# Kernel tuning notes

Hardware: AMD Instinct MI355X
Metric: run time of the kernel (lower is better)

The kernel has to match this reference:

```python
import jax, jax.numpy as jnp
import numpy as np

GROUP = 64   # quantization group size (nunchaku W4A4 default)
QMAX = 7.0   # symmetric int4 positive range


def setup_inputs() -> dict:
    key = jax.random.key(0)
    ks = jax.random.split(key, 6)
    T, K, N, R = 256, 3072, 3072, 32
    x = jax.random.normal(ks[0], (T, K), dtype=jnp.float32)
    # int4 weight codes stored as 0..15 (dequant subtracts zero-point 8)
    qweight = jax.random.randint(ks[1], (N, K), 0, 16, dtype=jnp.int32)
    # per-(out_channel, input_group) weight scales, small positive
    wscales = jax.random.uniform(ks[2], (N, K // GROUP), dtype=jnp.float32) * 0.02 + 1e-3
    lora_down = jax.random.normal(ks[3], (R, K), dtype=jnp.float32) / np.sqrt(K)
    lora_up = jax.random.normal(ks[4], (N, R), dtype=jnp.float32) / np.sqrt(R)
    bias = jax.random.normal(ks[5], (N,), dtype=jnp.float32) * 0.01
    return {"x": x, "qweight": qweight, "wscales": wscales,
            "lora_down": lora_down, "lora_up": lora_up, "bias": bias}


def _quantize_act(x):
    # per-token, per-group symmetric int4 fake-quant (quantize -> dequantize)
    T, K = x.shape
    xg = x.reshape(T, K // GROUP, GROUP)
    scale = jnp.maximum(jnp.max(jnp.abs(xg), axis=-1, keepdims=True) / QMAX, 1e-8)
    q = jnp.clip(jnp.round(xg / scale), -8.0, QMAX)
    return (q * scale).reshape(T, K)


def reference(x, qweight, wscales, lora_down, lora_up, bias):
    # Dequantize int4 weights: (code - 8) * per-group scale  -> [N, K]
    N, K = qweight.shape
    w = (qweight.astype(jnp.float32) - 8.0).reshape(N, K // GROUP, GROUP)
    w = (w * wscales[:, :, None]).reshape(N, K)
    # W4A4 main path: int4-quantized activations x dequantized int4 weights
    x_dq = _quantize_act(x)
    main = x_dq @ w.T                               # [T, N]
    # fused low-rank (SVDQuant LoRA) branch on full-precision activations
    lora = (x @ lora_down.T) @ lora_up.T            # [T, R] @ [R, N]
    return main + lora + bias
```

## Files before the change

### kernel.cpp

```cpp
#include <hip/hip_runtime.h>
#include <stdint.h>

#define T_DIM 256
#define K_DIM 3072
#define N_DIM 3072
#define R_DIM 32
#define KG    48
#define NCHUNK 49
#define NSPLIT 8

typedef __bf16 bf16x8 __attribute__((ext_vector_type(8)));
typedef float  f32x4  __attribute__((ext_vector_type(4)));
typedef unsigned short u16x8 __attribute__((ext_vector_type(8)));

__device__ __forceinline__ unsigned short f2bf(float f) {
    unsigned u = __builtin_bit_cast(unsigned, f);
    unsigned rounding = 0x7FFFu + ((u >> 16) & 1u);
    return (unsigned short)((u + rounding) >> 16);
}

__device__ __forceinline__ bf16x8 cvt8(const float* p) {
    float4 lo = ((const float4*)p)[0], hi = ((const float4*)p)[1];
    u16x8 u;
    u[0] = f2bf(lo.x); u[1] = f2bf(lo.y); u[2] = f2bf(lo.z); u[3] = f2bf(lo.w);
    u[4] = f2bf(hi.x); u[5] = f2bf(hi.y); u[6] = f2bf(hi.z); u[7] = f2bf(hi.w);
    return __builtin_bit_cast(bf16x8, u);
}

__device__ __forceinline__ void glds16(const void* gptr, void* lptr) {
    __builtin_amdgcn_global_load_lds(
        (const __attribute__((address_space(1))) unsigned int*)gptr,
        (__attribute__((address_space(3))) unsigned int*)lptr,
        16, 0, 0);
}

__global__ void build_wtail(const float* __restrict__ lora_up,
                            unsigned short* __restrict__ Wt) {
    int idx = blockIdx.x * 256 + threadIdx.x;
    int n = idx >> 6, j = idx & 63;
    int nblk = n >> 6, nl = n & 63;
    float v = (j < R_DIM) ? lora_up[n * R_DIM + j] : 0.f;
    Wt[(((size_t)nblk * 8 + (j >> 3)) * 64 + nl) * 8 + (j & 7)] = f2bf(v);
}

__global__ __launch_bounds__(256) void quant_act(
        const float* __restrict__ x, unsigned short* __restrict__ Ap) {
    int widx = blockIdx.x * 4 + (threadIdx.x >> 6);
    int lane = threadIdx.x & 63;
    int t = widx / KG, g = widx % KG;
    float v = x[(size_t)t * K_DIM + g * 64 + lane];
    float a = fabsf(v);
    #pragma unroll
    for (int off = 32; off; off >>= 1) a = fmaxf(a, __shfl_xor(a, off));
    float scale = fmaxf(a / 7.0f, 1e-8f);
    float q = rintf(v / scale);
    q = fminf(fmaxf(q, -8.f), 7.f);
    Ap[(((size_t)g * 8 + (lane >> 3)) * 256 + t) * 8 + (lane & 7)] = f2bf(q * scale);
}

__global__ __launch_bounds__(256) void lora_mid(
        const float* __restrict__ x, const float* __restrict__ lora_down,
        float* __restrict__ Lm) {
    int lane = threadIdx.x & 63, wv = threadIdx.x >> 6;
    int mrow = lane & 15, quad = lane >> 4;
    int k0 = blockIdx.x * 32 + quad * 8;
    bf16x8 a[4], b[2];
    #pragma unroll
    for (int mt = 0; mt < 4; ++mt)
        a[mt] = cvt8(x + (size_t)(wv * 64 + mt * 16 + mrow) * K_DIM + k0);
    #pragma unroll
    for (int nt = 0; nt < 2; ++nt)
        b[nt] = cvt8(lora_down + (size_t)(nt * 16 + mrow) * K_DIM + k0);
    f32x4 acc[4][2];
    f32x4 zero = {0.f, 0.f, 0.f, 0.f};
    #pragma unroll
    for (int i = 0; i < 4; ++i) { acc[i][0] = zero; acc[i][1] = zero; }
    #pragma unroll
    for (int mt = 0; mt < 4; ++mt)
        #pragma unroll
        for (int nt = 0; nt < 2; ++nt)
            acc[mt][nt] = __builtin_amdgcn_mfma_f32_16x16x32_bf16(
                a[mt], b[nt], acc[mt][nt], 0, 0, 0);
    #pragma unroll
    for (int mt = 0; mt < 4; ++mt)
        #pragma unroll
        for (int nt = 0; nt < 2; ++nt)
            #pragma unroll
            for (int r = 0; r < 4; ++r)
                atomicAdd(&Lm[(size_t)(wv * 64 + mt * 16 + quad * 4 + r) * R_DIM
                              + nt * 16 + mrow], acc[mt][nt][r]);
}

__global__ void pack_lora(const float* __restrict__ Lm,
                          unsigned short* __restrict__ Ap) {
    int idx = blockIdx.x * 256 + threadIdx.x;
    int t = idx >> 6, j = idx & 63;
    float v = (j < R_DIM) ? Lm[t * R_DIM + j] : 0.f;
    Ap[((size_t)(384 + (j >> 3)) * 256 + t) * 8 + (j & 7)] = f2bf(v);
}

__global__ __launch_bounds__(256) void gemm_main(
        const uint4*          __restrict__ ApU,
        const int*            __restrict__ qweight,
        const float*          __restrict__ wscales,
        const uint4*          __restrict__ WtU,
        const float*          __restrict__ bias,
        float*                __restrict__ out) {
    __shared__ uint4 AsU[2][2048];
    __shared__ uint4 BsU[2][512];
    int nblk  = blockIdx.x;
    int split = blockIdx.y;
    int c0 = split * 6;
    int c1 = (split == NSPLIT - 1) ? NCHUNK : c0 + 6;
    int tid = threadIdx.x;
    int lane = tid & 63, wv = tid >> 6;
    int mrow = lane & 15, quad = lane >> 4;
    int n_row = tid >> 2, seg = tid & 3;
    const int nbase = nblk * 64;
    const int* qrow = qweight + (size_t)(nbase + n_row) * K_DIM + seg * 16;
    const float* wsrow = wscales + (size_t)(nbase + n_row) * KG;

    f32x4 acc[4][4];
    f32x4 zero = {0.f, 0.f, 0.f, 0.f};
    #pragma unroll
    for (int i = 0; i < 4; ++i)
        #pragma unroll
        for (int j = 0; j < 4; ++j) acc[i][j] = zero;

    int4 bc[2][4];
    float wsr[2];

    {
        const uint4* gA = ApU + (size_t)c0 * 2048;
        #pragma unroll
        for (int i = 0; i < 8; ++i)
            glds16(&gA[tid + i * 256], &AsU[0][tid + i * 256]);
        const int4* g0 = (const int4*)(qrow + c0 * 64);
        const int4* g1 = (const int4*)(qrow + (c0 + 1) * 64);
        #pragma unroll
        for (int i = 0; i < 4; ++i) { bc[0][i] = g0[i]; bc[1][i] = g1[i]; }
        wsr[0] = wsrow[c0];
        wsr[1] = wsrow[c0 + 1];
    }

    for (int kt = c0; kt < c1; ++kt) {
        int lc = kt - c0;
        int p = lc & 1;
        if (kt < 48) {
            float w = wsr[p];
            const int* ci = (const int*)bc[p];
            alignas(16) unsigned short wb[16];
            #pragma unroll
            for (int j = 0; j < 16; ++j) wb[j] = f2bf((float)(ci[j] - 8) * w);
            const uint4* w2 = (const uint4*)wb;
            BsU[p][(seg * 2 + 0) * 64 + n_row] = w2[0];
            BsU[p][(seg * 2 + 1) * 64 + n_row] = w2[1];
        }
        __syncthreads();
        if (kt + 2 < c1 && kt + 2 < 48) {
            const int4* gq = (const int4*)(qrow + (kt + 2) * 64);
            #pragma unroll
            for (int i = 0; i < 4; ++i) bc[p][i] = gq[i];
            wsr[p] = wsrow[kt + 2];
        }
        if (kt + 1 < c1) {
            const uint4* gA = ApU + (size_t)(kt + 1) * 2048;
            #pragma unroll
            for (int i = 0; i < 8; ++i)
                glds16(&gA[tid + i * 256], &AsU[p ^ 1][tid + i * 256]);
            if (kt + 1 == 48) {
                #pragma unroll
                for (int j = 0; j < 2; ++j)
                    glds16(&WtU[(size_t)nblk * 512 + tid + j * 256],
                           &BsU[p ^ 1][tid + j * 256]);
            }
        }
        #pragma unroll
        for (int ks8 = 0; ks8 < 8; ks8 += 4) {
            bf16x8 a[4], b[4];
            #pragma unroll
            for (int mt = 0; mt < 4; ++mt)
                a[mt] = *(const bf16x8*)&AsU[p][(quad + ks8) * 256 + wv * 64 + mt * 16 + mrow];
            #pragma unroll
            for (int nt = 0; nt < 4; ++nt)
                b[nt] = *(const bf16x8*)&BsU[p][(quad + ks8) * 64 + nt * 16 + mrow];
            #pragma unroll
            for (int mt = 0; mt < 4; ++mt)
                #pragma unroll
                for (int nt = 0; nt < 4; ++nt)
                    acc[mt][nt] = __builtin_amdgcn_mfma_f32_16x16x32_bf16(
                        a[mt], b[nt], acc[mt][nt], 0, 0, 0);
        }
    }
    #pragma unroll
    for (int nt = 0; nt < 4; ++nt) {
        int n = nbase + nt * 16 + mrow;
        float bv = (split == NSPLIT - 1) ? bias[n] : 0.f;
        #pragma unroll
        for (int mt = 0; mt < 4; ++mt) {
            int row0 = wv * 64 + mt * 16 + quad * 4;
            #pragma unroll
            for (int r = 0; r < 4; ++r)
                atomicAdd(&out[(size_t)(row0 + r) * N_DIM + n], acc[mt][nt][r] + bv);
        }
    }
}

extern "C" void kernel_launch(void* const* d_in, const int* in_sizes, int n_in,
                              void* d_out, int out_size, void* d_ws, size_t ws_size,
                              hipStream_t stream) {
    const float* x         = (const float*)d_in[0];
    const int*   qweight   = (const int*)d_in[1];
    const float* wscales   = (const float*)d_in[2];
    const float* lora_down = (const float*)d_in[3];
    const float* lora_up   = (const float*)d_in[4];
    const float* bias      = (const float*)d_in[5];
    float* out = (float*)d_out;

    char* wsp = (char*)d_ws;
    unsigned short* Ap = (unsigned short*)wsp;
    wsp += (size_t)NCHUNK * 2048 * 16;
    unsigned short* Wt = (unsigned short*)wsp;
    wsp += (size_t)48 * 512 * 16;
    float* Lm = (float*)wsp;

    hipMemsetAsync(d_out, 0, (size_t)T_DIM * N_DIM * sizeof(float), stream);
    hipMemsetAsync(Lm, 0, (size_t)T_DIM * R_DIM * sizeof(float), stream);
    build_wtail<<<(N_DIM * 64) / 256, 256, 0, stream>>>(lora_up, Wt);
    quant_act<<<(T_DIM * KG) / 4, 256, 0, stream>>>(x, Ap);
    lora_mid<<<K_DIM / 32, 256, 0, stream>>>(x, lora_down, Lm);
    pack_lora<<<(T_DIM * 64) / 256, 256, 0, stream>>>(Lm, Ap);
    gemm_main<<<dim3(48, NSPLIT), 256, 0, stream>>>(
        (const uint4*)Ap, qweight, wscales, (const uint4*)Wt, bias, out);
}
```

Before: 140.6 us.

## Pack int4 weights in a prepass, halve split-K, replace atomics with a reduce kernel

A new pre-kernel packs the int32 weight codes into 4-bit nibbles, so the GEMM reads one eighth of the weight bytes per chunk. The split-K factor drops from 8 to 4, and each split writes its own partial buffer, which a separate reduce kernel sums and adds bias to. This removes the output memset and the float atomics. In exchange the full 36MB int32 weight must still be read once per call by the packing kernel, and the extra partial buffers add write and read traffic plus two kernel launches.

```diff
diff --git a/kernel.cpp b/kernel.cpp
--- a/kernel.cpp
+++ b/kernel.cpp
@@ -7,7 +7,7 @@
 #define R_DIM 32
 #define KG    48
 #define NCHUNK 49
-#define NSPLIT 8
+#define NSPLIT 4
 
 typedef __bf16 bf16x8 __attribute__((ext_vector_type(8)));
 typedef float  f32x4  __attribute__((ext_vector_type(4)));
@@ -32,6 +32,18 @@
         (const __attribute__((address_space(1))) unsigned int*)gptr,
         (__attribute__((address_space(3))) unsigned int*)lptr,
         16, 0, 0);
+}
+
+__global__ __launch_bounds__(256) void pack_qw(
+        const int* __restrict__ q, unsigned* __restrict__ Qp) {
+    size_t i = (size_t)blockIdx.x * 256 + threadIdx.x;
+    const int4* p = (const int4*)(q + i * 8);
+    int4 a = p[0], b = p[1];
+    unsigned w = (unsigned)(a.x & 15)        | ((unsigned)(a.y & 15) << 4)
+               | ((unsigned)(a.z & 15) << 8) | ((unsigned)(a.w & 15) << 12)
+               | ((unsigned)(b.x & 15) << 16)| ((unsigned)(b.y & 15) << 20)
+               | ((unsigned)(b.z & 15) << 24)| ((unsigned)(b.w & 15) << 28);
+    Qp[i] = w;
 }
 
 __global__ void build_wtail(const float* __restrict__ lora_up,
@@ -100,24 +112,23 @@
 }
 
 __global__ __launch_bounds__(256) void gemm_main(
-        const uint4*          __restrict__ ApU,
-        const int*            __restrict__ qweight,
-        const float*          __restrict__ wscales,
-        const uint4*          __restrict__ WtU,
-        const float*          __restrict__ bias,
-        float*                __restrict__ out) {
+        const uint4*    __restrict__ ApU,
+        const unsigned* __restrict__ Qp,
+        const float*    __restrict__ wscales,
+        const uint4*    __restrict__ WtU,
+        float*          __restrict__ P) {
     __shared__ uint4 AsU[2][2048];
     __shared__ uint4 BsU[2][512];
     int nblk  = blockIdx.x;
     int split = blockIdx.y;
-    int c0 = split * 6;
-    int c1 = (split == NSPLIT - 1) ? NCHUNK : c0 + 6;
+    int c0 = split * 12;
+    int c1 = (split == NSPLIT - 1) ? NCHUNK : c0 + 12;
     int tid = threadIdx.x;
     int lane = tid & 63, wv = tid >> 6;
     int mrow = lane & 15, quad = lane >> 4;
     int n_row = tid >> 2, seg = tid & 3;
     const int nbase = nblk * 64;
-    const int* qrow = qweight + (size_t)(nbase + n_row) * K_DIM + seg * 16;
+    const unsigned* qprow = Qp + (size_t)(nbase + n_row) * (K_DIM / 8) + seg * 2;
     const float* wsrow = wscales + (size_t)(nbase + n_row) * KG;
 
     f32x4 acc[4][4];
@@ -127,7 +138,7 @@
         #pragma unroll
         for (int j = 0; j < 4; ++j) acc[i][j] = zero;
 
-    int4 bc[2][4];
+    uint2 ubc[2];
     float wsr[2];
 
     {
@@ -135,10 +146,8 @@
         #pragma unroll
         for (int i = 0; i < 8; ++i)
             glds16(&gA[tid + i * 256], &AsU[0][tid + i * 256]);
-        const int4* g0 = (const int4*)(qrow + c0 * 64);
-        const int4* g1 = (const int4*)(qrow + (c0 + 1) * 64);
-        #pragma unroll
-        for (int i = 0; i < 4; ++i) { bc[0][i] = g0[i]; bc[1][i] = g1[i]; }
+        ubc[0] = *(const uint2*)(qprow + c0 * 8);
+        ubc[1] = *(const uint2*)(qprow + (c0 + 1) * 8);
         wsr[0] = wsrow[c0];
         wsr[1] = wsrow[c0 + 1];
     }
@@ -148,19 +157,21 @@
         int p = lc & 1;
         if (kt < 48) {
             float w = wsr[p];
-            const int* ci = (const int*)bc[p];
+            unsigned u0 = ubc[p].x, u1 = ubc[p].y;
             alignas(16) unsigned short wb[16];
             #pragma unroll
-            for (int j = 0; j < 16; ++j) wb[j] = f2bf((float)(ci[j] - 8) * w);
+            for (int j = 0; j < 8; ++j)
+                wb[j] = f2bf((float)((int)((u0 >> (4 * j)) & 15u) - 8) * w);
+            #pragma unroll
+            for (int j = 0; j < 8; ++j)
+                wb[8 + j] = f2bf((float)((int)((u1 >> (4 * j)) & 15u) - 8) * w);
             const uint4* w2 = (const uint4*)wb;
             BsU[p][(seg * 2 + 0) * 64 + n_row] = w2[0];
             BsU[p][(seg * 2 + 1) * 64 + n_row] = w2[1];
         }
         __syncthreads();
         if (kt + 2 < c1 && kt + 2 < 48) {
-            const int4* gq = (const int4*)(qrow + (kt + 2) * 64);
-            #pragma unroll
-            for (int i = 0; i < 4; ++i) bc[p][i] = gq[i];
+            ubc[p] = *(const uint2*)(qprow + (kt + 2) * 8);
             wsr[p] = wsrow[kt + 2];
         }
         if (kt + 1 < c1) {
@@ -192,18 +203,33 @@
                         a[mt], b[nt], acc[mt][nt], 0, 0, 0);
         }
     }
+    float* Pp = P + (size_t)split * (T_DIM * N_DIM);
     #pragma unroll
     for (int nt = 0; nt < 4; ++nt) {
         int n = nbase + nt * 16 + mrow;
-        float bv = (split == NSPLIT - 1) ? bias[n] : 0.f;
         #pragma unroll
         for (int mt = 0; mt < 4; ++mt) {
             int row0 = wv * 64 + mt * 16 + quad * 4;
             #pragma unroll
             for (int r = 0; r < 4; ++r)
-                atomicAdd(&out[(size_t)(row0 + r) * N_DIM + n], acc[mt][nt][r] + bv);
+                Pp[(size_t)(row0 + r) * N_DIM + n] = acc[mt][nt][r];
         }
     }
+}
+
+__global__ __launch_bounds__(256) void reduce_out(
+        const float4* __restrict__ P, const float* __restrict__ bias,
+        float4* __restrict__ out) {
+    int i = blockIdx.x * 256 + threadIdx.x;
+    const int STRIDE = T_DIM * N_DIM / 4;
+    float4 s0 = P[i], s1 = P[i + STRIDE], s2 = P[i + 2 * STRIDE], s3 = P[i + 3 * STRIDE];
+    float4 bv = *(const float4*)&bias[(i * 4) % N_DIM];
+    float4 o;
+    o.x = s0.x + s1.x + s2.x + s3.x + bv.x;
+    o.y = s0.y + s1.y + s2.y + s3.y + bv.y;
+    o.z = s0.z + s1.z + s2.z + s3.z + bv.z;
+    o.w = s0.w + s1.w + s2.w + s3.w + bv.w;
+    out[i] = o;
 }
 
 extern "C" void kernel_launch(void* const* d_in, const int* in_sizes, int n_in,
@@ -215,7 +241,6 @@
     const float* lora_down = (const float*)d_in[3];
     const float* lora_up   = (const float*)d_in[4];
     const float* bias      = (const float*)d_in[5];
-    float* out = (float*)d_out;
 
     char* wsp = (char*)d_ws;
     unsigned short* Ap = (unsigned short*)wsp;
@@ -223,13 +248,19 @@
     unsigned short* Wt = (unsigned short*)wsp;
     wsp += (size_t)48 * 512 * 16;
     float* Lm = (float*)wsp;
-
-    hipMemsetAsync(d_out, 0, (size_t)T_DIM * N_DIM * sizeof(float), stream);
+    wsp += (size_t)T_DIM * R_DIM * 4;
+    unsigned* Qp = (unsigned*)wsp;
+    wsp += (size_t)N_DIM * (K_DIM / 8) * 4;
+    float* P = (float*)wsp;
+
     hipMemsetAsync(Lm, 0, (size_t)T_DIM * R_DIM * sizeof(float), stream);
+    pack_qw<<<(N_DIM * (K_DIM / 8)) / 256, 256, 0, stream>>>(qweight, Qp);
     build_wtail<<<(N_DIM * 64) / 256, 256, 0, stream>>>(lora_up, Wt);
     quant_act<<<(T_DIM * KG) / 4, 256, 0, stream>>>(x, Ap);
     lora_mid<<<K_DIM / 32, 256, 0, stream>>>(x, lora_down, Lm);
     pack_lora<<<(T_DIM * 64) / 256, 256, 0, stream>>>(Lm, Ap);
     gemm_main<<<dim3(48, NSPLIT), 256, 0, stream>>>(
-        (const uint4*)Ap, qweight, wscales, (const uint4*)Wt, bias, out);
-}
+        (const uint4*)Ap, Qp, wscales, (const uint4*)Wt, P);
+    reduce_out<<<(T_DIM * N_DIM / 4) / 256, 256, 0, stream>>>(
+        (const float4*)P, bias, (float4*)d_out);
+}
```

After: 131.1 us. -6.8%, faster.
